# Kernel tuning notes

Hardware: AMD Instinct MI355X
Metric: run time of the kernel (lower is better)

Reference implementation:

```python
import jax, jax.numpy as jnp
import numpy as np

B, L, D = 4, 2048, 1024
H = 16
DH = D // H  # 64


def setup_inputs() -> dict:
    key = jax.random.key(0)
    ks = jax.random.split(key, 12)
    inp = {
        "key": jax.random.normal(ks[0], (B, L, D), jnp.float32),
        "value": jax.random.normal(ks[1], (B, L, D), jnp.float32),
        "query": jax.random.normal(ks[2], (B, L, D), jnp.float32),
        # causal mask: True = masked out (matches masked_fill semantics)
        "mask": jnp.broadcast_to(jnp.triu(jnp.ones((L, L), jnp.bool_), k=1), (B, L, L)),
        "Wk": jax.random.normal(ks[3], (D, D), jnp.float32) * 0.02,
        "bk": jnp.zeros((D,), jnp.float32),
        "Wv": jax.random.normal(ks[4], (D, D), jnp.float32) * 0.02,
        "bv": jnp.zeros((D,), jnp.float32),
        "Wq": jax.random.normal(ks[5], (D, D), jnp.float32) * 0.02,
        "bq": jnp.zeros((D,), jnp.float32),
        "Wo": jax.random.normal(ks[6], (D, D), jnp.float32) * 0.02,
        "bo": jnp.zeros((D,), jnp.float32),
    }
    return inp


def _split_heads(x):
    # [B, L, D] -> [B, H, L, DH]
    b, l, _ = x.shape
    return x.reshape(b, l, H, DH).transpose(0, 2, 1, 3)


def reference(key, value, query, mask, Wk, bk, Wv, bv, Wq, bq, Wo, bo):
    b, lq, _ = query.shape
    k_up = _split_heads(key @ Wk + bk)      # [B,H,Lk,DH]
    v_up = _split_heads(value @ Wv + bv)    # [B,H,Lk,DH]
    q_up = _split_heads(query @ Wq + bq) / jnp.sqrt(jnp.float32(DH))
    scores = jnp.einsum("bhqd,bhkd->bhqk", q_up, k_up)
    scores = jnp.where(mask[:, None, :, :], jnp.float32(-1e18), scores)
    attn = jax.nn.softmax(scores, axis=-1)  # dropout = identity (eval)
    ctx = jnp.einsum("bhqk,bhkd->bhqd", attn, v_up)
    ctx = ctx.transpose(0, 2, 1, 3).reshape(b, lq, H * DH)
    output = ctx @ Wo + bo                  # [B,Lq,D]
    top_attn = attn[:, 0, :, :]             # [B,Lq,Lk]
    return output, top_attn
```

## Files before the change

kernel.cpp:

```cpp
#include <hip/hip_runtime.h>
#include <hip/hip_bf16.h>
#include <stdint.h>

typedef unsigned short u16;
typedef unsigned int u32;
typedef __attribute__((ext_vector_type(8))) short bf16x8;
typedef __attribute__((ext_vector_type(4))) float f32x4;
typedef __attribute__((address_space(1))) unsigned int as1u;
typedef __attribute__((address_space(3))) unsigned int as3u;

#define DEV __device__ __forceinline__

DEV u16 f2bf(float f) {
  union { float f; unsigned u; } v; v.f = f;
  unsigned r = v.u + 0x7FFFu + ((v.u >> 16) & 1u);
  return (u16)(r >> 16);
}

DEV u32 cvtpk(float lo, float hi) {
  u32 r;
  asm("v_cvt_pk_bf16_f32 %0, %1, %2" : "=v"(r) : "v"(lo), "v"(hi));
  return r;
}

DEV void gl_lds16(const void* g, void* l) {
  __builtin_amdgcn_global_load_lds(
      reinterpret_cast<as1u*>(reinterpret_cast<uintptr_t>(g)),
      reinterpret_cast<as3u*>(reinterpret_cast<uintptr_t>(l)), 16, 0, 0);
}

DEV int swzh(int r, int c) { return r * 64 + (c ^ ((r & 7) << 3)); }

DEV int xcdswz512(int bid) { return ((bid & 7) << 6) | (bid >> 3); }

__global__ __launch_bounds__(256) void cvt3_k(const float* __restrict__ I0,
                                              const float* __restrict__ I1,
                                              const float* __restrict__ I2,
                                              u16* __restrict__ O0,
                                              u16* __restrict__ O1,
                                              u16* __restrict__ O2) {
  const int z = blockIdx.z;
  const float* in = z == 0 ? I0 : z == 1 ? I1 : I2;
  u16* out = z == 0 ? O0 : z == 1 ? O1 : O2;
  const int idx = blockIdx.x * 256 + threadIdx.x;
#pragma unroll
  for (int j = 0; j < 8; ++j) {
    const int i = j * 262144 + idx;
    float4 x = ((const float4*)in)[i];
    uint2 p;
    p.x = cvtpk(x.x, x.y);
    p.y = cvtpk(x.z, x.w);
    ((uint2*)out)[i] = p;
  }
}

__global__ __launch_bounds__(256) void wtrans4_k(
    const float* __restrict__ W0, const float* __restrict__ W1,
    const float* __restrict__ W2, const float* __restrict__ W3,
    u16* __restrict__ T0, u16* __restrict__ T1, u16* __restrict__ T2,
    u16* __restrict__ T3) {
  const int z = blockIdx.z;
  const float* W = z == 0 ? W0 : z == 1 ? W1 : z == 2 ? W2 : W3;
  u16* Wt = z == 0 ? T0 : z == 1 ? T1 : z == 2 ? T2 : T3;
  __shared__ float t[64][65];
  const int tid = threadIdx.x;
  const int n0 = blockIdx.x * 64, k0 = blockIdx.y * 64;
  const int c = tid & 63, r4 = tid >> 6;
#pragma unroll
  for (int i = 0; i < 16; ++i) {
    int r = r4 * 16 + i;
    t[r][c] = W[(size_t)(k0 + r) * 1024 + n0 + c];
  }
  __syncthreads();
#pragma unroll
  for (int i = 0; i < 16; ++i) {
    int r = r4 * 16 + i;
    Wt[(size_t)(n0 + r) * 1024 + k0 + c] = f2bf(t[c][r]);
  }
}

__global__ __launch_bounds__(256) void qkvgemm_k(
    const u16* __restrict__ Akey, const u16* __restrict__ Aval,
    const u16* __restrict__ Aqry, const u16* __restrict__ BtK,
    const u16* __restrict__ BtV, const u16* __restrict__ BtQ,
    const float* __restrict__ bk, const float* __restrict__ bv,
    const float* __restrict__ bq, u16* __restrict__ Kup, u16* __restrict__ Vt,
    u16* __restrict__ Qup, float qscale) {
  constexpr int K = 1024;
  const int z = blockIdx.z;
  const u16* Ah = z == 0 ? Akey : z == 1 ? Aval : Aqry;
  const u16* Bt = z == 0 ? BtK : z == 1 ? BtV : BtQ;
  const float* bias = z == 0 ? bk : z == 1 ? bv : bq;
  u16* Cp = z == 0 ? Kup : z == 1 ? Vt : Qup;
  const float scale = z == 2 ? qscale : 1.0f;

  __shared__ alignas(16) char smem[65536];

  const int tid = threadIdx.x;
  const int lane = tid & 63, wid = tid >> 6;
  const int swz = xcdswz512(blockIdx.x);
  const int brow = (swz >> 3) * 128;
  const int bcol = (swz & 7) * 128;
  const int wr = (wid >> 1) * 64, wc = (wid & 1) * 64;

  f32x4 acc[4][4] = {};

  auto stage = [&](int kt, int buf) {
#pragma unroll
    for (int i = 0; i < 4; ++i) {
      int row = i * 32 + (tid >> 3);
      const int sc = ((tid & 7) ^ (row & 7)) << 3;
      gl_lds16(Ah + (size_t)(brow + row) * K + kt + sc,
               smem + buf * 32768 + i * 4096 + wid * 1024);
      gl_lds16(Bt + (size_t)(bcol + row) * K + kt + sc,
               smem + buf * 32768 + 16384 + i * 4096 + wid * 1024);
    }
  };

  stage(0, 0);
  __syncthreads();

  int cur = 0;
  for (int kt = 0; kt < K; kt += 64) {
    if (kt + 64 < K) stage(kt + 64, cur ^ 1);
    const u16* Ash = (const u16*)(smem + cur * 32768);
    const u16* Bs = (const u16*)(smem + cur * 32768 + 16384);
#pragma unroll
    for (int kk = 0; kk < 2; ++kk) {
      const int kcol = kk * 32 + (lane >> 4) * 8;
      bf16x8 a[4], bfr[4];
#pragma unroll
      for (int m = 0; m < 4; ++m)
        a[m] = *(const bf16x8*)(Ash + swzh(wr + m * 16 + (lane & 15), kcol));
#pragma unroll
      for (int n = 0; n < 4; ++n)
        bfr[n] = *(const bf16x8*)(Bs + swzh(wc + n * 16 + (lane & 15), kcol));
#pragma unroll
      for (int m = 0; m < 4; ++m)
#pragma unroll
        for (int n = 0; n < 4; ++n)
          acc[m][n] = __builtin_amdgcn_mfma_f32_16x16x32_bf16(
              a[m], bfr[n], acc[m][n], 0, 0, 0);
    }
    __syncthreads();
    cur ^= 1;
  }

  const int g = lane >> 4;
  if (z == 1) {
    u16* T = (u16*)smem;
#pragma unroll
    for (int m = 0; m < 4; ++m) {
      const int row0 = wr + m * 16 + g * 4;
#pragma unroll
      for (int n = 0; n < 4; ++n) {
        const int col = wc + n * 16 + (lane & 15);
        const float bv2 = bias[bcol + col];
        uint2 p;
        p.x = cvtpk(acc[m][n][0] + bv2, acc[m][n][1] + bv2);
        p.y = cvtpk(acc[m][n][2] + bv2, acc[m][n][3] + bv2);
        *(uint2*)((char*)T + col * 256 + ((row0 * 2) ^ ((col & 7) << 4))) = p;
      }
    }
    __syncthreads();
    const int bI = brow >> 11, l0 = brow & 2047;
#pragma unroll
    for (int i = 0; i < 8; ++i) {
      const int rr = i * 16 + (tid >> 4);
      const int xb = (tid & 15) * 16;
      uint4 v = *(uint4*)((char*)T + rr * 256 + (xb ^ ((rr & 7) << 4)));
      const int colg = bcol + rr;
      const int hh = colg >> 6, dh = colg & 63;
      *(uint4*)(&Cp[((size_t)((bI << 4) + hh) * 64 + dh) * 2048 + l0 +
                    (xb >> 1)]) = v;
    }
  } else {
#pragma unroll
    for (int m = 0; m < 4; ++m) {
      const int row0 = brow + wr + m * 16 + (g << 2);
#pragma unroll
      for (int n = 0; n < 4; ++n) {
        const int col = bcol + wc + n * 16 + (lane & 15);
        const float bv2 = bias[col];
        const int h = col >> 6, dh = col & 63;
#pragma unroll
        for (int r = 0; r < 4; ++r) {
          const int row = row0 + r;
          const float val = (acc[m][n][r] + bv2) * scale;
          const int b = row >> 11, l = row & 2047;
          Cp[((size_t)((b << 4) + h) * 2048 + l) * 64 + dh] = f2bf(val);
        }
      }
    }
  }
}

__global__ __launch_bounds__(256) void outgemm_k(const u16* __restrict__ Ah,
                                                 const u16* __restrict__ Bt,
                                                 const float* __restrict__ bias,
                                                 float* __restrict__ Cp) {
  constexpr int K = 1024;
  __shared__ alignas(16) char smem[65536];

  const int tid = threadIdx.x;
  const int lane = tid & 63, wid = tid >> 6;
  const int swz = xcdswz512(blockIdx.x);
  const int brow = (swz >> 3) * 128;
  const int bcol = (swz & 7) * 128;
  const int wr = (wid >> 1) * 64, wc = (wid & 1) * 64;

  f32x4 acc[4][4] = {};

  auto stage = [&](int kt, int buf) {
#pragma unroll
    for (int i = 0; i < 4; ++i) {
      int row = i * 32 + (tid >> 3);
      const int sc = ((tid & 7) ^ (row & 7)) << 3;
      gl_lds16(Ah + (size_t)(brow + row) * K + kt + sc,
               smem + buf * 32768 + i * 4096 + wid * 1024);
      gl_lds16(Bt + (size_t)(bcol + row) * K + kt + sc,
               smem + buf * 32768 + 16384 + i * 4096 + wid * 1024);
    }
  };

  stage(0, 0);
  __syncthreads();

  int cur = 0;
  for (int kt = 0; kt < K; kt += 64) {
    if (kt + 64 < K) stage(kt + 64, cur ^ 1);
    const u16* Ash = (const u16*)(smem + cur * 32768);
    const u16* Bs = (const u16*)(smem + cur * 32768 + 16384);
#pragma unroll
    for (int kk = 0; kk < 2; ++kk) {
      const int kcol = kk * 32 + (lane >> 4) * 8;
      bf16x8 a[4], bfr[4];
#pragma unroll
      for (int m = 0; m < 4; ++m)
        a[m] = *(const bf16x8*)(Ash + swzh(wr + m * 16 + (lane & 15), kcol));
#pragma unroll
      for (int n = 0; n < 4; ++n)
        bfr[n] = *(const bf16x8*)(Bs + swzh(wc + n * 16 + (lane & 15), kcol));
#pragma unroll
      for (int m = 0; m < 4; ++m)
#pragma unroll
        for (int n = 0; n < 4; ++n)
          acc[m][n] = __builtin_amdgcn_mfma_f32_16x16x32_bf16(
              a[m], bfr[n], acc[m][n], 0, 0, 0);
    }
    __syncthreads();
    cur ^= 1;
  }

#pragma unroll
  for (int m = 0; m < 4; ++m) {
    const int row0 = brow + wr + m * 16 + ((lane >> 4) << 2);
#pragma unroll
    for (int n = 0; n < 4; ++n) {
      const int col = bcol + wc + n * 16 + (lane & 15);
      const float bv2 = bias[col];
#pragma unroll
      for (int r = 0; r < 4; ++r)
        Cp[(size_t)(row0 + r) * 1024 + col] = acc[m][n][r] + bv2;
    }
  }
}

__global__ __launch_bounds__(512, 4) void attn_k(const u16* __restrict__ Q,
                                                 const u16* __restrict__ K,
                                                 const u16* __restrict__ Vt,
                                                 u16* __restrict__ ctx,
                                                 float2* __restrict__ stats) {
  const int tid = threadIdx.x, lane = tid & 63, wid = tid >> 6;
  const int bh = blockIdx.x;
  const int qt = 15 - (int)blockIdx.y;
  const int b = bh >> 4, h = bh & 15;
  const size_t base = (size_t)bh * 2048 * 64;

  __shared__ alignas(16) u16 Ks[2][8192], Vs[2][8192], Ps[8192];

  bf16x8 qf[2];
  {
    const u16* qp = Q + base +
                    (size_t)(qt * 128 + wid * 16 + (lane & 15)) * 64 +
                    ((lane >> 4) << 3);
    qf[0] = *(const bf16x8*)(qp);
    qf[1] = *(const bf16x8*)(qp + 32);
  }
  bf16x8 ones;
#pragma unroll
  for (int i = 0; i < 8; ++i) ones[i] = (short)0x3F80;

  const int srowK = tid >> 3;
  const int scolK = ((tid & 7) ^ (srowK & 7)) << 3;
  const int srowV = tid >> 4;
  const int scolV = ((tid & 15) ^ (srowV & 7)) << 3;
  auto stage = [&](int kt, int buf) {
#pragma unroll
    for (int i = 0; i < 2; ++i)
      gl_lds16(K + base + (size_t)(kt * 128 + i * 64 + srowK) * 64 + scolK,
               (char*)Ks + buf * 16384 + i * 8192 + tid * 16);
#pragma unroll
    for (int i = 0; i < 2; ++i)
      gl_lds16(Vt + base + (size_t)(i * 32 + srowV) * 2048 + kt * 128 + scolV,
               (char*)Vs + buf * 16384 + i * 8192 + tid * 16);
  };

  f32x4 acc_o[4] = {}, acc_l = {};
  float m_run = -1e30f;
  const int q = qt * 128 + wid * 16 + (lane & 15);
  const int g = lane >> 4;
  const int l7 = lane & 7;

  stage(0, 0);
  __syncthreads();

  int cur = 0;
  for (int kt = 0; kt <= qt; ++kt) {
    if (kt < qt) stage(kt + 1, cur ^ 1);

    f32x4 s[8] = {};
#pragma unroll
    for (int kk = 0; kk < 2; ++kk) {
      const int kcb = kk * 64 + g * 16;
#pragma unroll
      for (int n2 = 0; n2 < 8; ++n2) {
        const int row = n2 * 16 + (lane & 15);
        bf16x8 kf = *(const bf16x8*)((char*)Ks + cur * 16384 + row * 128 +
                                     (kcb ^ ((row & 7) << 4)));
        s[n2] = __builtin_amdgcn_mfma_f32_16x16x32_bf16(kf, qf[kk], s[n2],
                                                        0, 0, 0);
      }
    }

    if (kt == qt) {
      const int kb = kt * 128 + g * 4;
#pragma unroll
      for (int n2 = 0; n2 < 8; ++n2)
#pragma unroll
        for (int r = 0; r < 4; ++r)
          if (kb + n2 * 16 + r > q) s[n2][r] = -1e30f;
    }

    float mn0 = fmaxf(fmaxf(fmaxf(s[0][0], s[0][1]), fmaxf(s[0][2], s[0][3])),
                      fmaxf(fmaxf(s[1][0], s[1][1]), fmaxf(s[1][2], s[1][3])));
    float mn1 = fmaxf(fmaxf(fmaxf(s[2][0], s[2][1]), fmaxf(s[2][2], s[2][3])),
                      fmaxf(fmaxf(s[3][0], s[3][1]), fmaxf(s[3][2], s[3][3])));
    float mn2 = fmaxf(fmaxf(fmaxf(s[4][0], s[4][1]), fmaxf(s[4][2], s[4][3])),
                      fmaxf(fmaxf(s[5][0], s[5][1]), fmaxf(s[5][2], s[5][3])));
    float mn3 = fmaxf(fmaxf(fmaxf(s[6][0], s[6][1]), fmaxf(s[6][2], s[6][3])),
                      fmaxf(fmaxf(s[7][0], s[7][1]), fmaxf(s[7][2], s[7][3])));
    float mx = fmaxf(fmaxf(mn0, mn1), fmaxf(mn2, mn3));
    mx = fmaxf(mx, __shfl_xor(mx, 16, 64));
    mx = fmaxf(mx, __shfl_xor(mx, 32, 64));

    if (__any(mx - m_run > 8.0f)) {
      const float mn = fmaxf(m_run, mx);
      const float alpha = exp2f(m_run - mn);
      m_run = mn;
#pragma unroll
      for (int r = 0; r < 4; ++r) {
        const float ar = __shfl(alpha, (g << 2) + r, 64);
        acc_l[r] *= ar;
#pragma unroll
        for (int n = 0; n < 4; ++n) acc_o[n][r] *= ar;
      }
    }

#pragma unroll
    for (int n2 = 0; n2 < 8; ++n2)
#pragma unroll
      for (int r = 0; r < 4; ++r) s[n2][r] = exp2f(s[n2][r] - m_run);

#pragma unroll
    for (int hf = 0; hf < 2; ++hf) {
#pragma unroll
      for (int n3 = 0; n3 < 4; ++n3) {
        const int n2 = hf * 4 + n3;
        union { u32 w[2]; uint2 u; } pk;
        pk.w[0] = cvtpk(s[n2][0], s[n2][1]);
        pk.w[1] = cvtpk(s[n2][2], s[n2][3]);
        *(uint2*)((char*)Ps + wid * 2048 + (lane & 15) * 128 +
                  ((n3 * 32 + g * 8) ^ (l7 << 4))) = pk.u;
      }
#pragma unroll
      for (int kk2 = 0; kk2 < 2; ++kk2) {
        bf16x8 pf = *(const bf16x8*)((char*)Ps + wid * 2048 +
                                     (lane & 15) * 128 +
                                     ((kk2 * 64 + g * 16) ^ (l7 << 4)));
        const int kvb = hf * 128 + kk2 * 64 + g * 16;
#pragma unroll
        for (int n = 0; n < 4; ++n) {
          const int dh = n * 16 + (lane & 15);
          bf16x8 vf = *(const bf16x8*)((char*)Vs + cur * 16384 + dh * 256 +
                                       (kvb ^ ((dh & 7) << 4)));
          acc_o[n] = __builtin_amdgcn_mfma_f32_16x16x32_bf16(pf, vf, acc_o[n],
                                                             0, 0, 0);
        }
        acc_l = __builtin_amdgcn_mfma_f32_16x16x32_bf16(pf, ones, acc_l,
                                                        0, 0, 0);
      }
    }
    __syncthreads();
    cur ^= 1;
  }

#pragma unroll
  for (int r = 0; r < 4; ++r) {
    const float linv = 1.0f / acc_l[r];
    const int qo = qt * 128 + wid * 16 + (g << 2) + r;
#pragma unroll
    for (int n = 0; n < 4; ++n) {
      const int dh = n * 16 + (lane & 15);
      ctx[((size_t)(b * 2048 + qo)) * 1024 + h * 64 + dh] =
          f2bf(acc_o[n][r] * linv);
    }
  }
  if (h == 0) {
    float mr[4];
#pragma unroll
    for (int r = 0; r < 4; ++r) mr[r] = __shfl(m_run, (g << 2) + r, 64);
    if ((lane & 15) == 0) {
#pragma unroll
      for (int r = 0; r < 4; ++r) {
        const int qo = qt * 128 + wid * 16 + (g << 2) + r;
        stats[b * 2048 + qo] = make_float2(mr[r], acc_l[r]);
      }
    }
  }
}

__global__ __launch_bounds__(256) void probs_k(const u16* __restrict__ Q,
                                               const u16* __restrict__ K,
                                               const float2* __restrict__ stats,
                                               float* __restrict__ out) {
  const int tid = threadIdx.x, lane = tid & 63, wid = tid >> 6;
  const int kt2 = blockIdx.x, qt = blockIdx.y, b = blockIdx.z;
  const int q0 = qt * 64, c0 = kt2 * 128;
  float* ot = out + ((size_t)b * 2048 + q0) * 2048 + c0;

  if (c0 > q0 + 63) {
    const float4 z = make_float4(0.f, 0.f, 0.f, 0.f);
#pragma unroll
    for (int i = 0; i < 8; ++i) {
      const int idx = i * 256 + tid;
      *(float4*)(ot + (size_t)(idx >> 5) * 2048 + ((idx & 31) << 2)) = z;
    }
    return;
  }

  __shared__ alignas(16) u16 Qs[4096], Ks2[8192];
  const size_t base = (size_t)(b * 16) * 2048 * 64;
#pragma unroll
  for (int i = 0; i < 2; ++i) {
    int row = i * 32 + (tid >> 3);
    gl_lds16(Q + base + (size_t)(q0 + row) * 64 + (((tid & 7) ^ (row & 7)) << 3),
             (char*)Qs + i * 4096 + wid * 1024);
  }
#pragma unroll
  for (int i = 0; i < 4; ++i) {
    int row = i * 32 + (tid >> 3);
    gl_lds16(K + base + (size_t)(c0 + row) * 64 + (((tid & 7) ^ (row & 7)) << 3),
             (char*)Ks2 + i * 4096 + wid * 1024);
  }
  __syncthreads();

  f32x4 s[8] = {};
#pragma unroll
  for (int kk = 0; kk < 2; ++kk) {
    const int kc = kk * 32 + (lane >> 4) * 8;
    bf16x8 aq = *(const bf16x8*)(Qs + swzh(wid * 16 + (lane & 15), kc));
#pragma unroll
    for (int n = 0; n < 8; ++n) {
      bf16x8 bk = *(const bf16x8*)(Ks2 + swzh(n * 16 + (lane & 15), kc));
      s[n] = __builtin_amdgcn_mfma_f32_16x16x32_bf16(aq, bk, s[n], 0, 0, 0);
    }
  }

#pragma unroll
  for (int r = 0; r < 4; ++r) {
    const int q = q0 + wid * 16 + ((lane >> 4) << 2) + r;
    const float2 st = stats[b * 2048 + q];
    const float rl = 1.0f / st.y;
#pragma unroll
    for (int n = 0; n < 8; ++n) {
      const int kp = c0 + n * 16 + (lane & 15);
      out[((size_t)b * 2048 + q) * 2048 + kp] =
          (kp <= q) ? exp2f(s[n][r] - st.x) * rl : 0.f;
    }
  }
}

extern "C" void kernel_launch(void* const* d_in, const int* in_sizes, int n_in,
                              void* d_out, int out_size, void* d_ws,
                              size_t ws_size, hipStream_t stream) {
  (void)in_sizes; (void)n_in; (void)out_size; (void)ws_size;
  const float* key = (const float*)d_in[0];
  const float* value = (const float*)d_in[1];
  const float* query = (const float*)d_in[2];
  const float* Wk = (const float*)d_in[4];
  const float* bk = (const float*)d_in[5];
  const float* Wv = (const float*)d_in[6];
  const float* bv = (const float*)d_in[7];
  const float* Wq = (const float*)d_in[8];
  const float* bq = (const float*)d_in[9];
  const float* Wo = (const float*)d_in[10];
  const float* bo = (const float*)d_in[11];

  char* ws = (char*)d_ws;
  u16* WtK = (u16*)(ws);
  u16* WtV = (u16*)(ws + (2u << 20));
  u16* WtQ = (u16*)(ws + (4u << 20));
  u16* WtO = (u16*)(ws + (6u << 20));
  u16* Kup = (u16*)(ws + (8u << 20));
  u16* Qup = (u16*)(ws + (24u << 20));
  u16* Vt  = (u16*)(ws + (40u << 20));
  u16* ctx = (u16*)(ws + (56u << 20));
  float2* stats = (float2*)(ws + (72u << 20));
  u16* Akb = (u16*)(ws + (76u << 20));
  u16* Avb = (u16*)(ws + (92u << 20));
  u16* Aqb = (u16*)(ws + (108u << 20));

  wtrans4_k<<<dim3(16, 16, 4), 256, 0, stream>>>(Wk, Wv, Wq, Wo, WtK, WtV,
                                                 WtQ, WtO);
  cvt3_k<<<dim3(1024, 1, 3), 256, 0, stream>>>(key, value, query, Akb, Avb,
                                               Aqb);

  const float qscale = 0.125f * 1.44269504088896340736f;
  qkvgemm_k<<<dim3(512, 1, 3), 256, 0, stream>>>(
      Akb, Avb, Aqb, WtK, WtV, WtQ, bk, bv, bq, Kup, Vt, Qup, qscale);

  attn_k<<<dim3(64, 16), 512, 0, stream>>>(Qup, Kup, Vt, ctx, stats);

  float* out = (float*)d_out;
  probs_k<<<dim3(16, 32, 4), 256, 0, stream>>>(Qup, Kup, stats,
                                               out + (size_t)8388608);

  outgemm_k<<<512, 256, 0, stream>>>(ctx, WtO, bo, out);
}
```

Measured before the change: 203.6 us.

## Fuse fp32-to-bf16 input conversion into QKV GEMM, add setprio, coalesce probs stores

Removes the separate cvt3_k pass. The QKV GEMM now loads fp32 activations into registers and converts them to bf16 while writing the swizzled LDS tile, which saves a full round trip of bf16 activations through global memory. It also wraps the MFMA sections of the attention kernel in s_setprio hints, and stages the probability tile through swizzled LDS so output rows go out as coalesced float4 stores. The cost is register-staged A loads (more VGPRs, no direct-to-LDS loads for A) and an extra barrier in probs_k.

```diff
diff --git a/kernel.cpp b/kernel.cpp
--- a/kernel.cpp
+++ b/kernel.cpp
@@ -32,27 +32,6 @@
 DEV int swzh(int r, int c) { return r * 64 + (c ^ ((r & 7) << 3)); }
 
 DEV int xcdswz512(int bid) { return ((bid & 7) << 6) | (bid >> 3); }
-
-__global__ __launch_bounds__(256) void cvt3_k(const float* __restrict__ I0,
-                                              const float* __restrict__ I1,
-                                              const float* __restrict__ I2,
-                                              u16* __restrict__ O0,
-                                              u16* __restrict__ O1,
-                                              u16* __restrict__ O2) {
-  const int z = blockIdx.z;
-  const float* in = z == 0 ? I0 : z == 1 ? I1 : I2;
-  u16* out = z == 0 ? O0 : z == 1 ? O1 : O2;
-  const int idx = blockIdx.x * 256 + threadIdx.x;
-#pragma unroll
-  for (int j = 0; j < 8; ++j) {
-    const int i = j * 262144 + idx;
-    float4 x = ((const float4*)in)[i];
-    uint2 p;
-    p.x = cvtpk(x.x, x.y);
-    p.y = cvtpk(x.z, x.w);
-    ((uint2*)out)[i] = p;
-  }
-}
 
 __global__ __launch_bounds__(256) void wtrans4_k(
     const float* __restrict__ W0, const float* __restrict__ W1,
@@ -80,15 +59,15 @@
 }
 
 __global__ __launch_bounds__(256) void qkvgemm_k(
-    const u16* __restrict__ Akey, const u16* __restrict__ Aval,
-    const u16* __restrict__ Aqry, const u16* __restrict__ BtK,
+    const float* __restrict__ Akey, const float* __restrict__ Aval,
+    const float* __restrict__ Aqry, const u16* __restrict__ BtK,
     const u16* __restrict__ BtV, const u16* __restrict__ BtQ,
     const float* __restrict__ bk, const float* __restrict__ bv,
     const float* __restrict__ bq, u16* __restrict__ Kup, u16* __restrict__ Vt,
     u16* __restrict__ Qup, float qscale) {
   constexpr int K = 1024;
   const int z = blockIdx.z;
-  const u16* Ah = z == 0 ? Akey : z == 1 ? Aval : Aqry;
+  const float* Af = z == 0 ? Akey : z == 1 ? Aval : Aqry;
   const u16* Bt = z == 0 ? BtK : z == 1 ? BtV : BtQ;
   const float* bias = z == 0 ? bk : z == 1 ? bv : bq;
   u16* Cp = z == 0 ? Kup : z == 1 ? Vt : Qup;
@@ -103,26 +82,51 @@
   const int bcol = (swz & 7) * 128;
   const int wr = (wid >> 1) * 64, wc = (wid & 1) * 64;
 
+  const int arow = tid >> 1, acol0 = (tid & 1) * 32;
+
   f32x4 acc[4][4] = {};
-
-  auto stage = [&](int kt, int buf) {
+  float4 fl[8];
+
+  auto loadA = [&](int kt) {
+    const float4* p =
+        (const float4*)(Af + (size_t)(brow + arow) * K + kt + acol0);
+#pragma unroll
+    for (int i = 0; i < 8; ++i) fl[i] = p[i];
+  };
+  auto writeA = [&](int buf) {
+    char* dst = smem + buf * 32768 + arow * 128;
+#pragma unroll
+    for (int i = 0; i < 4; ++i) {
+      uint4 v;
+      v.x = cvtpk(fl[2 * i].x, fl[2 * i].y);
+      v.y = cvtpk(fl[2 * i].z, fl[2 * i].w);
+      v.z = cvtpk(fl[2 * i + 1].x, fl[2 * i + 1].y);
+      v.w = cvtpk(fl[2 * i + 1].z, fl[2 * i + 1].w);
+      *(uint4*)(dst + ((acol0 * 2 + i * 16) ^ ((arow & 7) << 4))) = v;
+    }
+  };
+  auto stageB = [&](int kt, int buf) {
 #pragma unroll
     for (int i = 0; i < 4; ++i) {
       int row = i * 32 + (tid >> 3);
       const int sc = ((tid & 7) ^ (row & 7)) << 3;
-      gl_lds16(Ah + (size_t)(brow + row) * K + kt + sc,
-               smem + buf * 32768 + i * 4096 + wid * 1024);
       gl_lds16(Bt + (size_t)(bcol + row) * K + kt + sc,
                smem + buf * 32768 + 16384 + i * 4096 + wid * 1024);
     }
   };
 
-  stage(0, 0);
+  loadA(0);
+  stageB(0, 0);
+  writeA(0);
   __syncthreads();
 
   int cur = 0;
   for (int kt = 0; kt < K; kt += 64) {
-    if (kt + 64 < K) stage(kt + 64, cur ^ 1);
+    const bool next = (kt + 64 < K);
+    if (next) {
+      loadA(kt + 64);
+      stageB(kt + 64, cur ^ 1);
+    }
     const u16* Ash = (const u16*)(smem + cur * 32768);
     const u16* Bs = (const u16*)(smem + cur * 32768 + 16384);
 #pragma unroll
@@ -142,6 +146,7 @@
           acc[m][n] = __builtin_amdgcn_mfma_f32_16x16x32_bf16(
               a[m], bfr[n], acc[m][n], 0, 0, 0);
     }
+    if (next) writeA(cur ^ 1);
     __syncthreads();
     cur ^= 1;
   }
@@ -320,6 +325,7 @@
     if (kt < qt) stage(kt + 1, cur ^ 1);
 
     f32x4 s[8] = {};
+    __builtin_amdgcn_s_setprio(1);
 #pragma unroll
     for (int kk = 0; kk < 2; ++kk) {
       const int kcb = kk * 64 + g * 16;
@@ -332,6 +338,7 @@
                                                         0, 0, 0);
       }
     }
+    __builtin_amdgcn_s_setprio(0);
 
     if (kt == qt) {
       const int kb = kt * 128 + g * 4;
@@ -372,6 +379,7 @@
 #pragma unroll
       for (int r = 0; r < 4; ++r) s[n2][r] = exp2f(s[n2][r] - m_run);
 
+    __builtin_amdgcn_s_setprio(1);
 #pragma unroll
     for (int hf = 0; hf < 2; ++hf) {
 #pragma unroll
@@ -401,6 +409,7 @@
                                                         0, 0, 0);
       }
     }
+    __builtin_amdgcn_s_setprio(0);
     __syncthreads();
     cur ^= 1;
   }
@@ -449,7 +458,11 @@
     return;
   }
 
-  __shared__ alignas(16) u16 Qs[4096], Ks2[8192];
+  __shared__ alignas(16) char sm[32768];
+  u16* Qs = (u16*)sm;
+  u16* Ks2 = (u16*)(sm + 8192);
+  float* Pt = (float*)sm;
+
   const size_t base = (size_t)(b * 16) * 2048 * 64;
 #pragma unroll
   for (int i = 0; i < 2; ++i) {
@@ -476,18 +489,31 @@
       s[n] = __builtin_amdgcn_mfma_f32_16x16x32_bf16(aq, bk, s[n], 0, 0, 0);
     }
   }
+  __syncthreads();
 
 #pragma unroll
   for (int r = 0; r < 4; ++r) {
-    const int q = q0 + wid * 16 + ((lane >> 4) << 2) + r;
-    const float2 st = stats[b * 2048 + q];
+    const int ql = wid * 16 + ((lane >> 4) << 2) + r;
+    const int qg = q0 + ql;
+    const float2 st = stats[b * 2048 + qg];
     const float rl = 1.0f / st.y;
 #pragma unroll
     for (int n = 0; n < 8; ++n) {
-      const int kp = c0 + n * 16 + (lane & 15);
-      out[((size_t)b * 2048 + q) * 2048 + kp] =
-          (kp <= q) ? exp2f(s[n][r] - st.x) * rl : 0.f;
-    }
+      const int kp = n * 16 + (lane & 15);
+      const float v = (c0 + kp <= qg) ? exp2f(s[n][r] - st.x) * rl : 0.f;
+      Pt[ql * 128 + (kp ^ ((ql & 7) << 2))] = v;
+    }
+  }
+  __syncthreads();
+
+  const int rr = tid >> 2;
+  const int c00 = (tid & 3) * 32;
+  float* orow = out + ((size_t)b * 2048 + q0 + rr) * 2048 + c0 + c00;
+#pragma unroll
+  for (int j = 0; j < 8; ++j) {
+    const int c = c00 + j * 4;
+    float4 v = *(float4*)&Pt[rr * 128 + (c ^ ((rr & 7) << 2))];
+    *(float4*)(orow + j * 4) = v;
   }
 }
 
@@ -517,18 +543,13 @@
   u16* Vt  = (u16*)(ws + (40u << 20));
   u16* ctx = (u16*)(ws + (56u << 20));
   float2* stats = (float2*)(ws + (72u << 20));
-  u16* Akb = (u16*)(ws + (76u << 20));
-  u16* Avb = (u16*)(ws + (92u << 20));
-  u16* Aqb = (u16*)(ws + (108u << 20));
 
   wtrans4_k<<<dim3(16, 16, 4), 256, 0, stream>>>(Wk, Wv, Wq, Wo, WtK, WtV,
                                                  WtQ, WtO);
-  cvt3_k<<<dim3(1024, 1, 3), 256, 0, stream>>>(key, value, query, Akb, Avb,
-                                               Aqb);
 
   const float qscale = 0.125f * 1.44269504088896340736f;
   qkvgemm_k<<<dim3(512, 1, 3), 256, 0, stream>>>(
-      Akb, Avb, Aqb, WtK, WtV, WtQ, bk, bv, bq, Kup, Vt, Qup, qscale);
+      key, value, query, WtK, WtV, WtQ, bk, bv, bq, Kup, Vt, Qup, qscale);
 
   attn_k<<<dim3(64, 16), 512, 0, stream>>>(Qup, Kup, Vt, ctx, stats);
 
```

Result: slower. 282.9 us (+38.9%).
